# Optimization experiments

Measured on AMD Instinct MI355X. Metric: run time of the kernel, lower is better.

## Reference

```python
import jax, jax.numpy as jnp
import numpy as np

B, H, W = 64, 256, 256
G = 64
V = G * G          # 4096
HID = 512
S = 50


def _conv(x, w, b):
    # x: (B,C,H,W), w: (O,I,3,3) -> 'same' conv, NCHW
    y = jax.lax.conv_general_dilated(x, w, (1, 1), 'SAME',
                                     dimension_numbers=('NCHW', 'OIHW', 'NCHW'))
    return y + b[None, :, None, None]


def setup_inputs() -> dict:
    key = jax.random.key(0)
    ks = jax.random.split(key, 14)

    def lin(k, shape, fan_in):
        return (jax.random.normal(k, shape, jnp.float32) / np.float32(np.sqrt(fan_in)))

    return {
        'mask': jax.random.uniform(ks[0], (B, 1, H, W), jnp.float32),
        'target_ids': jax.random.randint(ks[1], (B, S), 0, V),
        'conv1_w': lin(ks[2], (16, 1, 3, 3), 9), 'conv1_b': jnp.zeros((16,), jnp.float32),
        'conv2_w': lin(ks[3], (32, 16, 3, 3), 16 * 9), 'conv2_b': jnp.zeros((32,), jnp.float32),
        'feat_w': lin(ks[4], (HID, 32), 32), 'feat_b': jnp.zeros((HID,), jnp.float32),
        'ctx_w': lin(ks[5], (HID, HID), HID), 'ctx_b': jnp.zeros((HID,), jnp.float32),
        'tok_emb': jax.random.normal(ks[6], (V + 1, HID), jnp.float32) * 0.02,
        'w_ih': lin(ks[7], (4 * HID, HID), HID), 'w_hh': lin(ks[8], (4 * HID, HID), HID),
        'b_ih': jnp.zeros((4 * HID,), jnp.float32), 'b_hh': jnp.zeros((4 * HID,), jnp.float32),
        'head_w': lin(ks[9], (V, HID), HID), 'head_b': jnp.zeros((V,), jnp.float32),
    }


def reference(mask, target_ids, conv1_w, conv1_b, conv2_w, conv2_b,
              feat_w, feat_b, ctx_w, ctx_b, tok_emb,
              w_ih, w_hh, b_ih, b_hh, head_w, head_b):
    b = mask.shape[0]
    vocab = head_w.shape[0]

    # --- CNN encoder ---
    x = jax.nn.relu(_conv(mask, conv1_w, conv1_b))                    # (B,16,H,W)
    x = jax.lax.reduce_window(x, -jnp.inf, jax.lax.max,
                              (1, 1, 2, 2), (1, 1, 2, 2), 'VALID')    # (B,16,H/2,W/2)
    x = jax.nn.relu(_conv(x, conv2_w, conv2_b))                       # (B,32,H/2,W/2)
    x = x.mean(axis=(2, 3))                                           # AdaptiveAvgPool2d(1) -> (B,32)

    h0 = x @ feat_w.T + feat_b                                        # (B,HID)
    c0 = jnp.zeros_like(h0)
    ctx = h0 @ ctx_w.T + ctx_b                                        # (B,HID)

    # Full teacher forcing (ratio=1.0): input token at t=0 is start token V,
    # at t>0 it is target_ids[:, t-1]. All embeddings gathered upfront.
    start = jnp.full((b, 1), vocab, dtype=target_ids.dtype)
    toks = jnp.concatenate([start, target_ids[:, :-1]], axis=1)       # (B,S)
    embs = tok_emb[toks]                                              # (B,S,HID)
    lstm_in = jnp.swapaxes(embs, 0, 1) + ctx[None]                    # (S,B,HID)

    bias = b_ih + b_hh

    def step(carry, inp):
        h, c = carry
        gates = inp @ w_ih.T + h @ w_hh.T + bias                      # (B,4*HID)
        i, f, g, o = jnp.split(gates, 4, axis=-1)
        c = jax.nn.sigmoid(f) * c + jax.nn.sigmoid(i) * jnp.tanh(g)
        h = jax.nn.sigmoid(o) * jnp.tanh(c)
        logit = h @ head_w.T + head_b                                 # (B,V)
        return (h, c), logit

    _, logits = jax.lax.scan(step, (h0, c0), lstm_in)                 # (S,B,V)
    return jnp.swapaxes(logits, 0, 1)                                 # (B,S,V)
```

## Files before the change

### kernel.cpp

```cpp
#include <hip/hip_runtime.h>
#include <cmath>

typedef __attribute__((ext_vector_type(8))) _Float16 f16x8;
typedef __attribute__((ext_vector_type(2))) _Float16 f16x2;
typedef __attribute__((ext_vector_type(4))) float f32x4;
typedef __attribute__((ext_vector_type(4))) unsigned u32x4;

#define LSTM_NB 32

__device__ __forceinline__ unsigned short f2h(float x) {
  return __builtin_bit_cast(unsigned short, (_Float16)x);
}

__device__ __forceinline__ float dot2(unsigned a, unsigned b, float c) {
#if __has_builtin(__builtin_amdgcn_fdot2)
  return __builtin_amdgcn_fdot2(__builtin_bit_cast(f16x2, a),
                                __builtin_bit_cast(f16x2, b), c, false);
#else
  f16x2 av = __builtin_bit_cast(f16x2, a), bv = __builtin_bit_cast(f16x2, b);
  return fmaf((float)av[0], (float)bv[0], fmaf((float)av[1], (float)bv[1], c));
#endif
}

__device__ __forceinline__ void gload16(const void* g, void* l) {
  __builtin_amdgcn_global_load_lds(
      (const __attribute__((address_space(1))) void*)g,
      (__attribute__((address_space(3))) void*)l, 16, 0, 0);
}

__device__ __forceinline__ void cload16(const void* p, u32x4* dst) {
  asm volatile("global_load_dwordx4 %0, %1, off sc0 sc1"
               : "=v"(*dst)
               : "v"(p));
}

__global__ __launch_bounds__(512) void k_conv(
    const float* __restrict__ mask, const float* __restrict__ w1,
    const float* __restrict__ b1, const float* __restrict__ w2,
    const float* __restrict__ b2, float* __restrict__ part)
{
  __shared__ unsigned s_p1p[8][18 * 36];
  __shared__ unsigned s_w2p[32][8][9];
  __shared__ float s_w1[144];
  __shared__ float s_b1[16];
  __shared__ float s_b2[32];

  const int tid = threadIdx.x;
  const int b = blockIdx.x >> 5;
  const int tile = blockIdx.x & 31;
  const int px0 = (tile & 3) * 32, py0 = (tile >> 2) * 16;
  const float* mb = mask + (size_t)b * 65536;

  for (int i = tid; i < 144; i += 512) s_w1[i] = w1[i];
  for (int i = tid; i < 2304; i += 512) {
    int oc = i / 72, p8 = (i % 72) / 9, k = i % 9;
    unsigned lo = f2h(w2[(size_t)(oc * 16 + 2 * p8) * 9 + k]);
    unsigned hi = f2h(w2[(size_t)(oc * 16 + 2 * p8 + 1) * 9 + k]);
    s_w2p[oc][p8][k] = lo | (hi << 16);
  }
  if (tid < 16) s_b1[tid] = b1[tid];
  if (tid < 32) s_b2[tid] = b2[tid];
  __syncthreads();

  for (int idx = tid; idx < 18 * 34; idx += 512) {
    int ly = idx / 34, lx = idx - ly * 34;
    int py = py0 - 1 + ly, px = px0 - 1 + lx;
    if (py < 0 || py >= 128 || px < 0 || px >= 128) {
      for (int p8 = 0; p8 < 8; p8++) s_p1p[p8][ly * 36 + lx] = 0;
    } else {
      float patch[4][4];
      int gy0 = 2 * py - 1, gx0 = 2 * px - 1;
#pragma unroll
      for (int i = 0; i < 4; i++) {
        int gy = gy0 + i;
        bool yok = (gy >= 0 && gy < 256);
#pragma unroll
        for (int j = 0; j < 4; j++) {
          int gx = gx0 + j;
          patch[i][j] = (yok && gx >= 0 && gx < 256) ? mb[gy * 256 + gx] : 0.f;
        }
      }
      float m[16];
      for (int o = 0; o < 16; o++) {
        float mm = 0.f;
#pragma unroll
        for (int dy = 0; dy < 2; dy++)
#pragma unroll
          for (int dx = 0; dx < 2; dx++) {
            float v = s_b1[o];
#pragma unroll
            for (int ky = 0; ky < 3; ky++)
#pragma unroll
              for (int kx = 0; kx < 3; kx++)
                v = fmaf(patch[dy + ky][dx + kx], s_w1[o * 9 + ky * 3 + kx], v);
            mm = fmaxf(mm, v);
          }
        m[o] = mm;
      }
#pragma unroll
      for (int p8 = 0; p8 < 8; p8++)
        s_p1p[p8][ly * 36 + lx] =
            (unsigned)f2h(m[2 * p8]) | ((unsigned)f2h(m[2 * p8 + 1]) << 16);
    }
  }
  __syncthreads();

  const int ocg = tid >> 6;
  const int sp = tid & 63;
  const int sx = (sp & 7) * 4, sy = (sp >> 3) * 2;
  float acc[4][8];
#pragma unroll
  for (int a = 0; a < 4; a++)
#pragma unroll
    for (int q = 0; q < 8; q++) acc[a][q] = 0.f;

  for (int p8 = 0; p8 < 8; p8++) {
    unsigned pp[4][6];
#pragma unroll
    for (int i = 0; i < 4; i++) {
      const unsigned* row = &s_p1p[p8][(sy + i) * 36 + sx];
#pragma unroll
      for (int j = 0; j < 6; j++) pp[i][j] = row[j];
    }
#pragma unroll
    for (int o4 = 0; o4 < 4; o4++) {
      const unsigned* w = &s_w2p[ocg * 4 + o4][p8][0];
      unsigned w00 = w[0], w01 = w[1], w02 = w[2];
      unsigned w10 = w[3], w11 = w[4], w12 = w[5];
      unsigned w20 = w[6], w21 = w[7], w22 = w[8];
#pragma unroll
      for (int y = 0; y < 2; y++)
#pragma unroll
        for (int x = 0; x < 4; x++) {
          float s = acc[o4][y * 4 + x];
          s = dot2(pp[y][x], w00, s);
          s = dot2(pp[y][x + 1], w01, s);
          s = dot2(pp[y][x + 2], w02, s);
          s = dot2(pp[y + 1][x], w10, s);
          s = dot2(pp[y + 1][x + 1], w11, s);
          s = dot2(pp[y + 1][x + 2], w12, s);
          s = dot2(pp[y + 2][x], w20, s);
          s = dot2(pp[y + 2][x + 1], w21, s);
          s = dot2(pp[y + 2][x + 2], w22, s);
          acc[o4][y * 4 + x] = s;
        }
    }
  }

  const int lane = tid & 63;
#pragma unroll
  for (int o4 = 0; o4 < 4; o4++) {
    float bv = s_b2[ocg * 4 + o4];
    float s = 0.f;
#pragma unroll
    for (int q = 0; q < 8; q++) s += fmaxf(acc[o4][q] + bv, 0.f);
    for (int off = 32; off > 0; off >>= 1) s += __shfl_down(s, off, 64);
    if (lane == 0) part[(b * 32 + tile) * 32 + ocg * 4 + o4] = s;
  }
}

__global__ __launch_bounds__(256) void k_pool_ctx(
    const float* __restrict__ part, const float* __restrict__ feat_w,
    const float* __restrict__ feat_b, const float* __restrict__ ctx_w,
    const float* __restrict__ ctx_b, float* __restrict__ h0,
    unsigned short* __restrict__ h0f, float* __restrict__ ctx)
{
  const int b = blockIdx.x, tid = threadIdx.x;
  __shared__ float pl[32];
  __shared__ float hs[512];
  if (tid < 32) {
    float s = 0.f;
    for (int t = 0; t < 32; t++) s += part[(b * 32 + t) * 32 + tid];
    pl[tid] = s * (1.0f / 16384.0f);
  }
  __syncthreads();
  for (int j = tid; j < 512; j += 256) {
    float acc = feat_b[j];
    const float* w = feat_w + j * 32;
#pragma unroll
    for (int ic = 0; ic < 32; ic++) acc = fmaf(pl[ic], w[ic], acc);
    h0[b * 512 + j] = acc;
    h0f[b * 512 + j] = f2h(acc);
    hs[j] = acc;
  }
  __syncthreads();
  for (int j = tid; j < 512; j += 256) {
    const float* w = ctx_w + (size_t)j * 512;
    float s0 = 0.f, s1 = 0.f, s2 = 0.f, s3 = 0.f;
    for (int k = 0; k < 512; k += 4) {
      float4 w4 = *(const float4*)(w + k);
      s0 = fmaf(hs[k], w4.x, s0);
      s1 = fmaf(hs[k + 1], w4.y, s1);
      s2 = fmaf(hs[k + 2], w4.z, s2);
      s3 = fmaf(hs[k + 3], w4.w, s3);
    }
    ctx[b * 512 + j] = ctx_b[j] + ((s0 + s1) + (s2 + s3));
  }
}

__global__ __launch_bounds__(256) void k_prep(
    const float* __restrict__ wih, const float* __restrict__ hw,
    unsigned short* __restrict__ wihb, unsigned short* __restrict__ hwb,
    int* __restrict__ flags)
{
  const int i = blockIdx.x * 256 + threadIdx.x;
  if (i < 1600) flags[i] = 0;
  if (i < 262144) {
    float4 v = *(const float4*)(wih + (size_t)i * 4);
    unsigned lo = (unsigned)f2h(v.x) | ((unsigned)f2h(v.y) << 16);
    unsigned hi = (unsigned)f2h(v.z) | ((unsigned)f2h(v.w) << 16);
    *(uint2*)(wihb + (size_t)i * 4) = make_uint2(lo, hi);
  } else if (i < 786432) {
    const int j = i - 262144;
    float4 v = *(const float4*)(hw + (size_t)j * 4);
    unsigned lo = (unsigned)f2h(v.x) | ((unsigned)f2h(v.y) << 16);
    unsigned hi = (unsigned)f2h(v.z) | ((unsigned)f2h(v.w) << 16);
    *(uint2*)(hwb + (size_t)j * 4) = make_uint2(lo, hi);
  }
}

__global__ __launch_bounds__(256) void k_zero_f(float* __restrict__ p) {
  p[blockIdx.x * 256 + threadIdx.x] = 0.f;
}

__global__ __launch_bounds__(128) void k_build_A(
    const float* __restrict__ tok_emb, const int* __restrict__ tgt,
    const float* __restrict__ ctx, unsigned short* __restrict__ A)
{
  const int r = blockIdx.x;
  const int t = r >> 6, b = r & 63;
  const int tok = (t == 0) ? 4096 : tgt[b * 50 + (t - 1)];
  const int i = threadIdx.x * 4;
  float4 ev = *(const float4*)(tok_emb + (size_t)tok * 512 + i);
  float4 cv = *(const float4*)(ctx + b * 512 + i);
  unsigned lo = (unsigned)f2h(ev.x + cv.x) | ((unsigned)f2h(ev.y + cv.y) << 16);
  unsigned hi = (unsigned)f2h(ev.z + cv.z) | ((unsigned)f2h(ev.w + cv.w) << 16);
  *(uint2*)(A + (size_t)r * 512 + i) = make_uint2(lo, hi);
}

template <int MODE>
__global__ __launch_bounds__(256) void k_gemm_mfma(
    const unsigned short* __restrict__ A, const unsigned short* __restrict__ B,
    const float* __restrict__ bias_a, const float* __restrict__ bias_b,
    float* __restrict__ C, int NB)
{
  __shared__ unsigned short sA[128 * 32];
  __shared__ unsigned short sB[128 * 32];
  const int tid = threadIdx.x;
  const int bx = blockIdx.x % NB, by = blockIdx.x / NB;
  const int lane = tid & 63, wv = tid >> 6;
  const int wr = wv >> 1, wc = wv & 1;
  const unsigned short* Ab = A + (size_t)by * 128 * 512;
  const unsigned short* Bb = B + (size_t)bx * 128 * 512;

  f32x4 acc[4][4];
#pragma unroll
  for (int m = 0; m < 4; m++)
#pragma unroll
    for (int n = 0; n < 4; n++) acc[m][n] = (f32x4){0.f, 0.f, 0.f, 0.f};

  const int r0 = tid >> 2, c0 = (tid & 3) * 8;
  const int idx1 = tid + 256;
  const int r1 = idx1 >> 2, c1 = (idx1 & 3) * 8;
  unsigned short* lA0 = sA + (size_t)wv * 512;
  unsigned short* lA1 = sA + 2048 + (size_t)wv * 512;
  unsigned short* lB0 = sB + (size_t)wv * 512;
  unsigned short* lB1 = sB + 2048 + (size_t)wv * 512;

  const int frow = lane & 15;
  const int foff = (lane >> 4) * 8;

  for (int kc = 0; kc < 512; kc += 32) {
    gload16(Ab + (size_t)r0 * 512 + kc + c0, lA0);
    gload16(Ab + (size_t)r1 * 512 + kc + c1, lA1);
    gload16(Bb + (size_t)r0 * 512 + kc + c0, lB0);
    gload16(Bb + (size_t)r1 * 512 + kc + c1, lB1);
    __syncthreads();

    f16x8 af[4], bfr[4];
#pragma unroll
    for (int m = 0; m < 4; m++)
      af[m] = *(const f16x8*)(sA + (wr * 64 + m * 16 + frow) * 32 + foff);
#pragma unroll
    for (int n = 0; n < 4; n++)
      bfr[n] = *(const f16x8*)(sB + (wc * 64 + n * 16 + frow) * 32 + foff);
#pragma unroll
    for (int m = 0; m < 4; m++)
#pragma unroll
      for (int n = 0; n < 4; n++)
        acc[m][n] = __builtin_amdgcn_mfma_f32_16x16x32_f16(
            af[m], bfr[n], acc[m][n], 0, 0, 0);
    __syncthreads();
  }

#pragma unroll
  for (int n = 0; n < 4; n++) {
    const int gc = bx * 128 + wc * 64 + n * 16 + (lane & 15);
    const float bv = (MODE == 0) ? (bias_a[gc] + bias_b[gc]) : bias_a[gc];
#pragma unroll
    for (int m = 0; m < 4; m++) {
      const int rb = by * 128 + wr * 64 + m * 16 + (lane >> 4) * 4;
#pragma unroll
      for (int j = 0; j < 4; j++) {
        const int r = rb + j;
        float v = acc[m][n][j] + bv;
        int t = r >> 6, bb = r & 63;
        if (MODE == 0) {
          C[(size_t)t * 131072 + (size_t)gc * 64 + bb] = v;
        } else {
          C[((size_t)bb * 50 + t) * 4096 + gc] = v;
        }
      }
    }
  }
}

__global__ __launch_bounds__(256, 1) void k_lstm_mfma(
    const float* __restrict__ xgT,
    const float* __restrict__ w_hh,
    const unsigned short* __restrict__ h0f,
    unsigned short* __restrict__ hallf,
    int* __restrict__ flags)
{
  __shared__ unsigned short s_h[64 * 512];
  __shared__ float s_g[4][64][17];
  const int tid = threadIdx.x;
  const int kb = blockIdx.x;
  const int g = tid >> 6;
  const int lane = tid & 63;
  const int frow = lane & 15;
  const int foff = (lane >> 4) * 8;

  f16x8 wf[16];
  {
    const float* wrow = w_hh + (size_t)(g * 512 + kb * 16 + frow) * 512;
#pragma unroll
    for (int kf = 0; kf < 16; kf++) {
      float tmp[8];
      *(float4*)tmp = *(const float4*)(wrow + kf * 32 + foff);
      *(float4*)(tmp + 4) = *(const float4*)(wrow + kf * 32 + foff + 4);
#pragma unroll
      for (int j = 0; j < 8; j++) wf[kf][j] = (_Float16)tmp[j];
    }
  }

  float c[4] = {0.f, 0.f, 0.f, 0.f};
  const int b2 = tid & 63, dd2 = tid >> 6;

  for (int t = 0; t < 50; ++t) {
    const unsigned short* H = t ? hallf + (size_t)(t - 1) * 32768 : h0f;

    const float* xr =
        xgT + (size_t)t * 131072 + (size_t)(kb * 16 + dd2 * 4) * 64 + b2;
    float xv[16];
#pragma unroll
    for (int gq = 0; gq < 4; gq++)
#pragma unroll
      for (int i = 0; i < 4; i++)
        xv[gq * 4 + i] = xr[(size_t)(gq * 512 + i) * 64];

    if (t > 0 && tid < 32) {
      while (__hip_atomic_load(&flags[(t - 1) * 32 + tid], __ATOMIC_RELAXED,
                               __HIP_MEMORY_SCOPE_AGENT) == 0) {
        __builtin_amdgcn_s_sleep(1);
      }
    }
    __syncthreads();

    {
      u32x4 r[16];
#pragma unroll
      for (int i = 0; i < 16; i++)
        cload16((const char*)H + (size_t)(tid + i * 256) * 16, &r[i]);
      asm volatile("s_waitcnt vmcnt(0)" ::: "memory");
      __builtin_amdgcn_sched_barrier(0);
#pragma unroll
      for (int i = 0; i < 16; i++) {
        int byte = (tid + i * 256) * 16;
        int swz = byte ^ (((byte >> 10) & 7) << 4);
        *(u32x4*)((char*)s_h + swz) = r[i];
      }
    }
    __syncthreads();

    f32x4 acc[4];
#pragma unroll
    for (int mt = 0; mt < 4; mt++) acc[mt] = (f32x4){0.f, 0.f, 0.f, 0.f};
#pragma unroll
    for (int kf = 0; kf < 16; kf++) {
#pragma unroll
      for (int mt = 0; mt < 4; mt++) {
        const int row = mt * 16 + frow;
        const int byte = (row << 10) + kf * 64 + foff * 2;
        const int swz = byte ^ ((row & 7) << 4);
        f16x8 ah = *(const f16x8*)((const char*)s_h + swz);
        acc[mt] =
            __builtin_amdgcn_mfma_f32_16x16x32_f16(ah, wf[kf], acc[mt], 0, 0, 0);
      }
    }
#pragma unroll
    for (int mt = 0; mt < 4; mt++)
#pragma unroll
      for (int j = 0; j < 4; j++)
        s_g[g][mt * 16 + (lane >> 4) * 4 + j][frow] = acc[mt][j];
    __syncthreads();

    unsigned long long qf = 0;
#pragma unroll
    for (int i = 0; i < 4; i++) {
      float gi = s_g[0][b2][dd2 * 4 + i] + xv[0 + i];
      float gf = s_g[1][b2][dd2 * 4 + i] + xv[4 + i];
      float gg = s_g[2][b2][dd2 * 4 + i] + xv[8 + i];
      float go = s_g[3][b2][dd2 * 4 + i] + xv[12 + i];
      float ig = 1.f / (1.f + expf(-gi));
      float fg = 1.f / (1.f + expf(-gf));
      float og = 1.f / (1.f + expf(-go));
      float gt = tanhf(gg);
      c[i] = fmaf(fg, c[i], ig * gt);
      float h = og * tanhf(c[i]);
      qf |= (unsigned long long)f2h(h) << (16 * i);
    }
    const size_t ho = (size_t)b2 * 512 + kb * 16 + dd2 * 4;
    __hip_atomic_store((unsigned long long*)(hallf + (size_t)t * 32768 + ho),
                       qf, __ATOMIC_RELAXED, __HIP_MEMORY_SCOPE_AGENT);
    __syncthreads();
    if (t < 49 && tid == 0)
      __hip_atomic_store(&flags[t * 32 + kb], 1, __ATOMIC_RELAXED,
                         __HIP_MEMORY_SCOPE_AGENT);
  }
}

__global__ __launch_bounds__(256) void k_lstm_step1(
    const float* __restrict__ xgT, const float* __restrict__ w_hh,
    const float* __restrict__ hin, float* __restrict__ hout,
    unsigned short* __restrict__ hallf_t, float* __restrict__ cbuf, int t)
{
  __shared__ float s_w[8][512];
  __shared__ float s_g[2][4][64];
  const int tid = threadIdx.x;
  const int dd0 = blockIdx.x * 2;

  for (int idx = tid; idx < 1024; idx += 256) {
    int row = idx >> 7;
    int k4 = (idx & 127) << 2;
    int q_ = row >> 1, dd_i = row & 1;
    *(float4*)&s_w[row][k4] =
        *(const float4*)(w_hh + (size_t)(q_ * 512 + dd0 + dd_i) * 512 + k4);
  }
  const int b = tid & 63;
  const int q = tid >> 6;
  __syncthreads();

  const float* hc = hin + b * 512;
  const float* xr = xgT + (size_t)t * 131072 + (size_t)(q * 512 + dd0) * 64 + b;
  float a0 = xr[0], a1 = xr[64];
  const float* w0 = s_w[q * 2 + 0];
  const float* w1 = s_w[q * 2 + 1];
#pragma unroll 8
  for (int k = 0; k < 512; k += 4) {
    float4 h4 = *(const float4*)(hc + k);
    float4 u = *(const float4*)(w0 + k);
    float4 v = *(const float4*)(w1 + k);
    a0 = fmaf(h4.x, u.x, fmaf(h4.y, u.y, fmaf(h4.z, u.z, fmaf(h4.w, u.w, a0))));
    a1 = fmaf(h4.x, v.x, fmaf(h4.y, v.y, fmaf(h4.z, v.z, fmaf(h4.w, v.w, a1))));
  }
  s_g[0][q][b] = a0;
  s_g[1][q][b] = a1;
  __syncthreads();
  if (q < 2) {
    const int dd = dd0 + q;
    float gi = s_g[q][0][b], gf = s_g[q][1][b];
    float gg = s_g[q][2][b], go = s_g[q][3][b];
    float ig = 1.f / (1.f + expf(-gi));
    float fg = 1.f / (1.f + expf(-gf));
    float og = 1.f / (1.f + expf(-go));
    float gt = tanhf(gg);
    float c = fmaf(fg, cbuf[b * 512 + dd], ig * gt);
    float h = og * tanhf(c);
    cbuf[b * 512 + dd] = c;
    hout[b * 512 + dd] = h;
    hallf_t[(size_t)b * 512 + dd] = f2h(h);
  }
}

extern "C" void kernel_launch(void* const* d_in, const int* in_sizes, int n_in,
                              void* d_out, int out_size, void* d_ws,
                              size_t ws_size, hipStream_t stream) {
  const float* mask   = (const float*)d_in[0];
  const int*   tgt    = (const int*)d_in[1];
  const float* w1     = (const float*)d_in[2];
  const float* b1     = (const float*)d_in[3];
  const float* w2     = (const float*)d_in[4];
  const float* b2     = (const float*)d_in[5];
  const float* feat_w = (const float*)d_in[6];
  const float* feat_b = (const float*)d_in[7];
  const float* ctx_w  = (const float*)d_in[8];
  const float* ctx_b  = (const float*)d_in[9];
  const float* temb   = (const float*)d_in[10];
  const float* w_ih   = (const float*)d_in[11];
  const float* w_hh_p = (const float*)d_in[12];
  const float* b_ih   = (const float*)d_in[13];
  const float* b_hh   = (const float*)d_in[14];
  const float* head_w = (const float*)d_in[15];
  const float* head_b = (const float*)d_in[16];

  float* ws = (float*)d_ws;
  float* part  = ws;
  float* hbuf  = ws + 65536;
  float* ctx   = ws + 131072;
  int*   flags = (int*)(ws + 163840);
  unsigned short* h0f  = (unsigned short*)(ws + 165440);
  unsigned short* Ab16 = (unsigned short*)(ws + 181824);
  unsigned short* hallf = Ab16;
  unsigned short* wihb = (unsigned short*)(ws + 1001024);
  unsigned short* hwb  = (unsigned short*)(ws + 1525312);
  float* xgT   = ws + 2573888;
  float* cbuf  = part;
  float* out   = (float*)d_out;

  k_conv<<<2048, 512, 0, stream>>>(mask, w1, b1, w2, b2, part);
  k_prep<<<3072, 256, 0, stream>>>(w_ih, head_w, wihb, hwb, flags);
  k_pool_ctx<<<64, 256, 0, stream>>>(part, feat_w, feat_b, ctx_w, ctx_b,
                                     hbuf, h0f, ctx);
  k_build_A<<<3200, 128, 0, stream>>>(temb, tgt, ctx, Ab16);
  k_gemm_mfma<0><<<25 * 16, 256, 0, stream>>>(Ab16, wihb, b_ih, b_hh, xgT, 16);

  {
    const float* xgT_c = xgT;
    const float* whh_c = w_hh_p;
    const unsigned short* h0f_c = h0f;
    unsigned short* hallf_c = hallf;
    int* flags_c = flags;
    void* args[] = {(void*)&xgT_c, (void*)&whh_c, (void*)&h0f_c,
                    (void*)&hallf_c, (void*)&flags_c};
    hipError_t e = hipLaunchCooperativeKernel(
        (const void*)k_lstm_mfma, dim3(LSTM_NB), dim3(256), args, 0, stream);
    if (e != hipSuccess) {
      (void)hipGetLastError();
      k_zero_f<<<128, 256, 0, stream>>>(cbuf);
      for (int t = 0; t < 50; t++) {
        const float* hin = hbuf + (t & 1) * 32768;
        float* hout = hbuf + ((t + 1) & 1) * 32768;
        k_lstm_step1<<<256, 256, 0, stream>>>(
            xgT, w_hh_p, hin, hout, hallf + (size_t)t * 32768, cbuf, t);
      }
    }
  }

  k_gemm_mfma<1><<<25 * 32, 256, 0, stream>>>(hallf, hwb, head_b, nullptr, out, 32);
}
```

Before: 510.6 us.

## Overlap output head GEMM with LSTM recurrence in one cooperative kernel

Adds 192 head blocks to the cooperative LSTM launch. Using per-timestep flags, they compute the vocabulary projection for finished timesteps while the 32 recurrence blocks keep stepping, so the head GEMM runs concurrently instead of afterwards. Separately, the conv kernel stages the mask tile in LDS as fp16 instead of issuing repeated global loads per pooled pixel. The overlap risks contention between head blocks and recurrence blocks for memory bandwidth. Head blocks also wait on flags up to eight steps ahead, which serializes part of their work, and the fp16 mask adds rounding error.

```diff
diff --git a/kernel.cpp b/kernel.cpp
--- a/kernel.cpp
+++ b/kernel.cpp
@@ -6,7 +6,8 @@
 typedef __attribute__((ext_vector_type(4))) float f32x4;
 typedef __attribute__((ext_vector_type(4))) unsigned u32x4;
 
-#define LSTM_NB 32
+#define REC_NB 32
+#define HEAD_NB 192
 
 __device__ __forceinline__ unsigned short f2h(float x) {
   return __builtin_bit_cast(unsigned short, (_Float16)x);
@@ -39,6 +40,7 @@
     const float* __restrict__ b1, const float* __restrict__ w2,
     const float* __restrict__ b2, float* __restrict__ part)
 {
+  __shared__ unsigned short s_mask[38 * 72];
   __shared__ unsigned s_p1p[8][18 * 36];
   __shared__ unsigned s_w2p[32][8][9];
   __shared__ float s_w1[144];
@@ -50,6 +52,7 @@
   const int tile = blockIdx.x & 31;
   const int px0 = (tile & 3) * 32, py0 = (tile >> 2) * 16;
   const float* mb = mask + (size_t)b * 65536;
+  const int gr0 = 2 * py0 - 3, gc0 = 2 * px0 - 3;
 
   for (int i = tid; i < 144; i += 512) s_w1[i] = w1[i];
   for (int i = tid; i < 2304; i += 512) {
@@ -60,6 +63,14 @@
   }
   if (tid < 16) s_b1[tid] = b1[tid];
   if (tid < 32) s_b2[tid] = b2[tid];
+
+  for (int idx = tid; idx < 38 * 70; idx += 512) {
+    int r = idx / 70, cc = idx - r * 70;
+    int gr = gr0 + r, gc = gc0 + cc;
+    float v = (gr >= 0 && gr < 256 && gc >= 0 && gc < 256)
+                  ? mb[gr * 256 + gc] : 0.f;
+    s_mask[r * 72 + cc] = f2h(v);
+  }
   __syncthreads();
 
   for (int idx = tid; idx < 18 * 34; idx += 512) {
@@ -69,17 +80,12 @@
       for (int p8 = 0; p8 < 8; p8++) s_p1p[p8][ly * 36 + lx] = 0;
     } else {
       float patch[4][4];
-      int gy0 = 2 * py - 1, gx0 = 2 * px - 1;
-#pragma unroll
-      for (int i = 0; i < 4; i++) {
-        int gy = gy0 + i;
-        bool yok = (gy >= 0 && gy < 256);
-#pragma unroll
-        for (int j = 0; j < 4; j++) {
-          int gx = gx0 + j;
-          patch[i][j] = (yok && gx >= 0 && gx < 256) ? mb[gy * 256 + gx] : 0.f;
-        }
-      }
+      const unsigned short* pm = &s_mask[(2 * ly) * 72 + 2 * lx];
+#pragma unroll
+      for (int i = 0; i < 4; i++)
+#pragma unroll
+        for (int j = 0; j < 4; j++)
+          patch[i][j] = (float)__builtin_bit_cast(_Float16, pm[i * 72 + j]);
       float m[16];
       for (int o = 0; o < 16; o++) {
         float mm = 0.f;
@@ -204,7 +210,7 @@
     int* __restrict__ flags)
 {
   const int i = blockIdx.x * 256 + threadIdx.x;
-  if (i < 1600) flags[i] = 0;
+  if (i < 6400) flags[i] = 0;
   if (i < 262144) {
     float4 v = *(const float4*)(wih + (size_t)i * 4);
     unsigned lo = (unsigned)f2h(v.x) | ((unsigned)f2h(v.y) << 16);
@@ -315,118 +321,188 @@
   }
 }
 
-__global__ __launch_bounds__(256, 1) void k_lstm_mfma(
+__global__ __launch_bounds__(256, 1) void k_lstm_head(
     const float* __restrict__ xgT,
     const float* __restrict__ w_hh,
     const unsigned short* __restrict__ h0f,
     unsigned short* __restrict__ hallf,
+    const unsigned short* __restrict__ hwb,
+    const float* __restrict__ head_b,
+    float* __restrict__ out,
     int* __restrict__ flags)
 {
   __shared__ unsigned short s_h[64 * 512];
   __shared__ float s_g[4][64][17];
   const int tid = threadIdx.x;
-  const int kb = blockIdx.x;
-  const int g = tid >> 6;
   const int lane = tid & 63;
   const int frow = lane & 15;
   const int foff = (lane >> 4) * 8;
 
-  f16x8 wf[16];
-  {
-    const float* wrow = w_hh + (size_t)(g * 512 + kb * 16 + frow) * 512;
-#pragma unroll
-    for (int kf = 0; kf < 16; kf++) {
-      float tmp[8];
-      *(float4*)tmp = *(const float4*)(wrow + kf * 32 + foff);
-      *(float4*)(tmp + 4) = *(const float4*)(wrow + kf * 32 + foff + 4);
-#pragma unroll
-      for (int j = 0; j < 8; j++) wf[kf][j] = (_Float16)tmp[j];
-    }
-  }
-
-  float c[4] = {0.f, 0.f, 0.f, 0.f};
-  const int b2 = tid & 63, dd2 = tid >> 6;
-
-  for (int t = 0; t < 50; ++t) {
-    const unsigned short* H = t ? hallf + (size_t)(t - 1) * 32768 : h0f;
-
-    const float* xr =
-        xgT + (size_t)t * 131072 + (size_t)(kb * 16 + dd2 * 4) * 64 + b2;
-    float xv[16];
-#pragma unroll
-    for (int gq = 0; gq < 4; gq++)
-#pragma unroll
-      for (int i = 0; i < 4; i++)
-        xv[gq * 4 + i] = xr[(size_t)(gq * 512 + i) * 64];
-
-    if (t > 0 && tid < 32) {
-      while (__hip_atomic_load(&flags[(t - 1) * 32 + tid], __ATOMIC_RELAXED,
-                               __HIP_MEMORY_SCOPE_AGENT) == 0) {
-        __builtin_amdgcn_s_sleep(1);
-      }
-    }
-    __syncthreads();
-
+  if (blockIdx.x < REC_NB) {
+    const int kb = blockIdx.x;
+    const int g = tid >> 6;
+
+    f16x8 wf[16];
     {
-      u32x4 r[16];
-#pragma unroll
-      for (int i = 0; i < 16; i++)
-        cload16((const char*)H + (size_t)(tid + i * 256) * 16, &r[i]);
-      asm volatile("s_waitcnt vmcnt(0)" ::: "memory");
-      __builtin_amdgcn_sched_barrier(0);
-#pragma unroll
-      for (int i = 0; i < 16; i++) {
-        int byte = (tid + i * 256) * 16;
-        int swz = byte ^ (((byte >> 10) & 7) << 4);
-        *(u32x4*)((char*)s_h + swz) = r[i];
-      }
-    }
-    __syncthreads();
-
-    f32x4 acc[4];
-#pragma unroll
-    for (int mt = 0; mt < 4; mt++) acc[mt] = (f32x4){0.f, 0.f, 0.f, 0.f};
-#pragma unroll
-    for (int kf = 0; kf < 16; kf++) {
-#pragma unroll
-      for (int mt = 0; mt < 4; mt++) {
-        const int row = mt * 16 + frow;
-        const int byte = (row << 10) + kf * 64 + foff * 2;
-        const int swz = byte ^ ((row & 7) << 4);
-        f16x8 ah = *(const f16x8*)((const char*)s_h + swz);
-        acc[mt] =
-            __builtin_amdgcn_mfma_f32_16x16x32_f16(ah, wf[kf], acc[mt], 0, 0, 0);
-      }
-    }
-#pragma unroll
-    for (int mt = 0; mt < 4; mt++)
-#pragma unroll
-      for (int j = 0; j < 4; j++)
-        s_g[g][mt * 16 + (lane >> 4) * 4 + j][frow] = acc[mt][j];
-    __syncthreads();
-
-    unsigned long long qf = 0;
-#pragma unroll
-    for (int i = 0; i < 4; i++) {
-      float gi = s_g[0][b2][dd2 * 4 + i] + xv[0 + i];
-      float gf = s_g[1][b2][dd2 * 4 + i] + xv[4 + i];
-      float gg = s_g[2][b2][dd2 * 4 + i] + xv[8 + i];
-      float go = s_g[3][b2][dd2 * 4 + i] + xv[12 + i];
-      float ig = 1.f / (1.f + expf(-gi));
-      float fg = 1.f / (1.f + expf(-gf));
-      float og = 1.f / (1.f + expf(-go));
-      float gt = tanhf(gg);
-      c[i] = fmaf(fg, c[i], ig * gt);
-      float h = og * tanhf(c[i]);
-      qf |= (unsigned long long)f2h(h) << (16 * i);
-    }
-    const size_t ho = (size_t)b2 * 512 + kb * 16 + dd2 * 4;
-    __hip_atomic_store((unsigned long long*)(hallf + (size_t)t * 32768 + ho),
-                       qf, __ATOMIC_RELAXED, __HIP_MEMORY_SCOPE_AGENT);
-    __syncthreads();
-    if (t < 49 && tid == 0)
-      __hip_atomic_store(&flags[t * 32 + kb], 1, __ATOMIC_RELAXED,
-                         __HIP_MEMORY_SCOPE_AGENT);
+      const float* wrow = w_hh + (size_t)(g * 512 + kb * 16 + frow) * 512;
+#pragma unroll
+      for (int kf = 0; kf < 16; kf++) {
+        float tmp[8];
+        *(float4*)tmp = *(const float4*)(wrow + kf * 32 + foff);
+        *(float4*)(tmp + 4) = *(const float4*)(wrow + kf * 32 + foff + 4);
+#pragma unroll
+        for (int j = 0; j < 8; j++) wf[kf][j] = (_Float16)tmp[j];
+      }
+    }
+
+    float c[4] = {0.f, 0.f, 0.f, 0.f};
+    const int b2 = tid & 63, dd2 = tid >> 6;
+
+    for (int t = 0; t < 50; ++t) {
+      const unsigned short* H = t ? hallf + (size_t)(t - 1) * 32768 : h0f;
+
+      const float* xr =
+          xgT + (size_t)t * 131072 + (size_t)(kb * 16 + dd2 * 4) * 64 + b2;
+      float xv[16];
+#pragma unroll
+      for (int gq = 0; gq < 4; gq++)
+#pragma unroll
+        for (int i = 0; i < 4; i++)
+          xv[gq * 4 + i] = xr[(size_t)(gq * 512 + i) * 64];
+
+      if (t > 0 && tid < 32) {
+        while (__hip_atomic_load(&flags[(t - 1) * 32 + tid], __ATOMIC_RELAXED,
+                                 __HIP_MEMORY_SCOPE_AGENT) == 0) {
+          __builtin_amdgcn_s_sleep(1);
+        }
+      }
+      __syncthreads();
+
+      {
+        u32x4 r[16];
+#pragma unroll
+        for (int i = 0; i < 16; i++)
+          cload16((const char*)H + (size_t)(tid + i * 256) * 16, &r[i]);
+        asm volatile("s_waitcnt vmcnt(0)" ::: "memory");
+        __builtin_amdgcn_sched_barrier(0);
+#pragma unroll
+        for (int i = 0; i < 16; i++) {
+          int byte = (tid + i * 256) * 16;
+          int swz = byte ^ (((byte >> 10) & 7) << 4);
+          *(u32x4*)((char*)s_h + swz) = r[i];
+        }
+      }
+      __syncthreads();
+
+      f32x4 acc[4];
+#pragma unroll
+      for (int mt = 0; mt < 4; mt++) acc[mt] = (f32x4){0.f, 0.f, 0.f, 0.f};
+#pragma unroll
+      for (int kf = 0; kf < 16; kf++) {
+#pragma unroll
+        for (int mt = 0; mt < 4; mt++) {
+          const int row = mt * 16 + frow;
+          const int byte = (row << 10) + kf * 64 + foff * 2;
+          const int swz = byte ^ ((row & 7) << 4);
+          f16x8 ah = *(const f16x8*)((const char*)s_h + swz);
+          acc[mt] = __builtin_amdgcn_mfma_f32_16x16x32_f16(ah, wf[kf],
+                                                           acc[mt], 0, 0, 0);
+        }
+      }
+#pragma unroll
+      for (int mt = 0; mt < 4; mt++)
+#pragma unroll
+        for (int j = 0; j < 4; j++)
+          s_g[g][mt * 16 + (lane >> 4) * 4 + j][frow] = acc[mt][j];
+      __syncthreads();
+
+      unsigned long long qf = 0;
+#pragma unroll
+      for (int i = 0; i < 4; i++) {
+        float gi = s_g[0][b2][dd2 * 4 + i] + xv[0 + i];
+        float gf = s_g[1][b2][dd2 * 4 + i] + xv[4 + i];
+        float gg = s_g[2][b2][dd2 * 4 + i] + xv[8 + i];
+        float go = s_g[3][b2][dd2 * 4 + i] + xv[12 + i];
+        float ig = 1.f / (1.f + expf(-gi));
+        float fg = 1.f / (1.f + expf(-gf));
+        float og = 1.f / (1.f + expf(-go));
+        float gt = tanhf(gg);
+        c[i] = fmaf(fg, c[i], ig * gt);
+        float h = og * tanhf(c[i]);
+        qf |= (unsigned long long)f2h(h) << (16 * i);
+      }
+      const size_t ho = (size_t)b2 * 512 + kb * 16 + dd2 * 4;
+      __hip_atomic_store((unsigned long long*)(hallf + (size_t)t * 32768 + ho),
+                         qf, __ATOMIC_RELAXED, __HIP_MEMORY_SCOPE_AGENT);
+      __syncthreads();
+      if (tid == 0)
+        __hip_atomic_store(&flags[t * 32 + kb], 1, __ATOMIC_RELAXED,
+                           __HIP_MEMORY_SCOPE_AGENT);
+    }
+  } else {
+    const int hb = blockIdx.x - REC_NB;
+    const int ct = hb % 64;
+    const int tg = hb / 64;
+    const int wv = tid >> 6;
+
+    f16x8 bf[16];
+    const unsigned short* brow =
+        hwb + (size_t)(ct * 64 + wv * 16 + frow) * 512;
+#pragma unroll
+    for (int kf = 0; kf < 16; kf++)
+      bf[kf] = *(const f16x8*)(brow + kf * 32 + foff);
+    const float bias = head_b[ct * 64 + wv * 16 + frow];
+
+    for (int t = tg; t < 50; t += 3) {
+      const int tw = (t + 8 > 49) ? 49 : t + 8;
+      if (tid < 32) {
+        while (__hip_atomic_load(&flags[tw * 32 + tid], __ATOMIC_RELAXED,
+                                 __HIP_MEMORY_SCOPE_AGENT) == 0) {
+          __builtin_amdgcn_s_sleep(16);
+        }
+      }
+      __syncthreads();
+
+      {
+        const u32x4* src = (const u32x4*)(hallf + (size_t)t * 32768);
+        u32x4 r[16];
+#pragma unroll
+        for (int i = 0; i < 16; i++) r[i] = src[tid + i * 256];
+#pragma unroll
+        for (int i = 0; i < 16; i++) {
+          int byte = (tid + i * 256) * 16;
+          int swz = byte ^ (((byte >> 10) & 7) << 4);
+          *(u32x4*)((char*)s_h + swz) = r[i];
+        }
+      }
+      __syncthreads();
+
+      f32x4 acc[4];
+#pragma unroll
+      for (int m = 0; m < 4; m++) acc[m] = (f32x4){0.f, 0.f, 0.f, 0.f};
+#pragma unroll
+      for (int kf = 0; kf < 16; kf++) {
+#pragma unroll
+        for (int m = 0; m < 4; m++) {
+          const int row = m * 16 + frow;
+          const int byte = (row << 10) + kf * 64 + foff * 2;
+          const int swz = byte ^ ((row & 7) << 4);
+          f16x8 ah = *(const f16x8*)((const char*)s_h + swz);
+          acc[m] = __builtin_amdgcn_mfma_f32_16x16x32_f16(ah, bf[kf], acc[m],
+                                                          0, 0, 0);
+        }
+      }
+      const int gc = ct * 64 + wv * 16 + (lane & 15);
+#pragma unroll
+      for (int m = 0; m < 4; m++) {
+#pragma unroll
+        for (int j = 0; j < 4; j++) {
+          const int b = m * 16 + (lane >> 4) * 4 + j;
+          out[((size_t)b * 50 + t) * 4096 + gc] = acc[m][j] + bias;
+        }
+      }
+      __syncthreads();
+    }
   }
 }
 
@@ -509,12 +585,12 @@
   float* hbuf  = ws + 65536;
   float* ctx   = ws + 131072;
   int*   flags = (int*)(ws + 163840);
-  unsigned short* h0f  = (unsigned short*)(ws + 165440);
-  unsigned short* Ab16 = (unsigned short*)(ws + 181824);
+  unsigned short* h0f  = (unsigned short*)(ws + 170240);
+  unsigned short* Ab16 = (unsigned short*)(ws + 186624);
   unsigned short* hallf = Ab16;
-  unsigned short* wihb = (unsigned short*)(ws + 1001024);
-  unsigned short* hwb  = (unsigned short*)(ws + 1525312);
-  float* xgT   = ws + 2573888;
+  unsigned short* wihb = (unsigned short*)(ws + 1005824);
+  unsigned short* hwb  = (unsigned short*)(ws + 1530112);
+  float* xgT   = ws + 2578688;
   float* cbuf  = part;
   float* out   = (float*)d_out;
 
@@ -530,11 +606,16 @@
     const float* whh_c = w_hh_p;
     const unsigned short* h0f_c = h0f;
     unsigned short* hallf_c = hallf;
+    const unsigned short* hwb_c = hwb;
+    const float* headb_c = head_b;
+    float* out_c = out;
     int* flags_c = flags;
-    void* args[] = {(void*)&xgT_c, (void*)&whh_c, (void*)&h0f_c,
-                    (void*)&hallf_c, (void*)&flags_c};
+    void* args[] = {(void*)&xgT_c,   (void*)&whh_c,  (void*)&h0f_c,
+                    (void*)&hallf_c, (void*)&hwb_c,  (void*)&headb_c,
+                    (void*)&out_c,   (void*)&flags_c};
     hipError_t e = hipLaunchCooperativeKernel(
-        (const void*)k_lstm_mfma, dim3(LSTM_NB), dim3(256), args, 0, stream);
+        (const void*)k_lstm_head, dim3(REC_NB + HEAD_NB), dim3(256), args, 0,
+        stream);
     if (e != hipSuccess) {
       (void)hipGetLastError();
       k_zero_f<<<128, 256, 0, stream>>>(cbuf);
@@ -544,8 +625,8 @@
         k_lstm_step1<<<256, 256, 0, stream>>>(
             xgT, w_hh_p, hin, hout, hallf + (size_t)t * 32768, cbuf, t);
       }
-    }
-  }
-
-  k_gemm_mfma<1><<<25 * 32, 256, 0, stream>>>(hallf, hwb, head_b, nullptr, out, 32);
-}
+      k_gemm_mfma<1><<<25 * 32, 256, 0, stream>>>(hallf, hwb, head_b, nullptr,
+                                                  out, 32);
+    }
+  }
+}
```

Measured after the change: 538.0 us. 1.05x slower.
